# Performance work log

Hardware: AMD Instinct MI355X
Metric: run time of the kernel (lower is better)

The kernel has to match this reference:

```python
import jax, jax.numpy as jnp
import numpy as np

H = 8       # n_heads
E = 128     # embedding_size (= per-head dim)
NEG = -1000000000.0


def setup_inputs() -> dict:
    key = jax.random.key(0)
    ks = jax.random.split(key, 12)
    b, n = 8, 1024
    x = jax.random.normal(ks[0], (b, n, E), dtype=jnp.float32)
    dist = jax.random.normal(ks[1], (b, n, n), dtype=jnp.float32)
    mask = jax.random.randint(ks[2], (b, n), 0, 2).astype(jnp.float32)
    s = 1.0 / np.sqrt(E)
    Wq = jax.random.normal(ks[3], (E, H * E), dtype=jnp.float32) * s
    Wk = jax.random.normal(ks[4], (E, H * E), dtype=jnp.float32) * s
    Wv = jax.random.normal(ks[5], (E, H * E), dtype=jnp.float32) * s
    bq = jnp.zeros((H * E,), jnp.float32)
    bk = jnp.zeros((H * E,), jnp.float32)
    bv = jnp.zeros((H * E,), jnp.float32)
    Wo = jax.random.normal(ks[6], (H * E, E), dtype=jnp.float32) * (1.0 / np.sqrt(H * E))
    bo = jnp.zeros((E,), jnp.float32)
    return {"x": x, "dist": dist, "mask": mask, "Wq": Wq, "bq": bq,
            "Wk": Wk, "bk": bk, "Wv": Wv, "bv": bv, "Wo": Wo, "bo": bo}


def reference(x, dist, mask, Wq, bq, Wk, bk, Wv, bv, Wo, bo):
    b, n, e = x.shape
    scale = e ** (-0.5)
    # project and split heads: [b, n, H*E] -> [b, H, n, E]
    def heads(W, bias):
        return (x @ W + bias).reshape(b, n, H, e).transpose(0, 2, 1, 3)
    q = heads(Wq, bq) * mask[:, None, :, None]
    k = heads(Wk, bk) * mask[:, None, :, None]
    v = heads(Wv, bv) * mask[:, None, :, None]
    # scores with additive distance bias broadcast over heads
    a = jnp.einsum('bhqe,bhke->bhqk', q * scale, k) + dist[:, None, :, :]
    am = jnp.einsum('bq,bk->bqk', mask, mask)[:, None, :, :]  # [b,1,n,n]
    a = jnp.where(am == 0, NEG, a)
    a = jax.nn.softmax(a, axis=-1)
    a = jnp.where(am == 0, 0.0, a)
    y = jnp.einsum('bhqk,bhke->bhqe', a, v)
    y = y.transpose(0, 2, 1, 3).reshape(b, n, H * e)
    y = y @ Wo + bo
    return y * mask[:, :, None]
```

## Files before the change

### kernel.cpp

```cpp
#include <hip/hip_runtime.h>
#include <hip/hip_bf16.h>
#include <hip/hip_fp16.h>

#define NH 8
#define ED 128
#define NB 8
#define NN 1024

typedef __attribute__((ext_vector_type(8))) short s16x8;
typedef __attribute__((ext_vector_type(8))) __bf16 bf16x8_t;
typedef __attribute__((ext_vector_type(4))) float f32x4;
typedef __attribute__((ext_vector_type(16))) float f32x16;
typedef __attribute__((ext_vector_type(4))) unsigned int u32x4;

#define LOG2E 1.4426950408889634f
#define SINIT -23.083120654223414f

static __device__ __forceinline__ unsigned short f2bf(float f) {
    union { float f; unsigned u; } v; v.f = f;
    unsigned r = v.u + 0x7fffu + ((v.u >> 16) & 1u);
    return (unsigned short)(r >> 16);
}

static __device__ __forceinline__ f32x4 mfma16(s16x8 a, s16x8 b, f32x4 c) {
    return __builtin_amdgcn_mfma_f32_16x16x32_bf16(
        __builtin_bit_cast(bf16x8_t, a), __builtin_bit_cast(bf16x8_t, b), c, 0, 0, 0);
}

static __device__ __forceinline__ f32x16 mfma32(s16x8 a, s16x8 b, f32x16 c) {
    return __builtin_amdgcn_mfma_f32_32x32x16_bf16(
        __builtin_bit_cast(bf16x8_t, a), __builtin_bit_cast(bf16x8_t, b), c, 0, 0, 0);
}

static __device__ __forceinline__ unsigned cvtpk(float lo, float hi) {
    unsigned r;
    asm("v_cvt_pk_bf16_f32 %0, %1, %2" : "=v"(r) : "v"(lo), "v"(hi));
    return r;
}

static __device__ __forceinline__ void gll16(const void* g, void* l) {
    __builtin_amdgcn_global_load_lds((const __attribute__((address_space(1))) void*)g,
                                     (__attribute__((address_space(3))) void*)l, 16, 0, 0);
}

__global__ __launch_bounds__(256) void prep_kernel(
    const float* __restrict__ x,
    const float* __restrict__ Wq, const float* __restrict__ Wk,
    const float* __restrict__ Wv, const float* __restrict__ Wo,
    const float* __restrict__ dist,
    const float* __restrict__ mask,
    unsigned short* __restrict__ xb,
    unsigned short* __restrict__ wqt, unsigned short* __restrict__ wkt,
    unsigned short* __restrict__ wvt, unsigned short* __restrict__ wot,
    unsigned short* __restrict__ dswz) {
    int bid = blockIdx.x, tid = threadIdx.x;

    if (bid < 1024) {
        int kt = bid & 15;
        int t = bid >> 4;
        int qt = t & 7;
        int b = t >> 3;

        __shared__ float dtile[128][65];
        __shared__ float mrow[64];

        {
            int seg = tid & 15;
            int r0 = tid >> 4;
            const float* src = dist + ((size_t)b * NN + qt * 128) * NN + kt * 64;
#pragma unroll
            for (int pass = 0; pass < 8; ++pass) {
                int row = pass * 16 + r0;
                f32x4 v = *(const f32x4*)(src + (size_t)row * NN + seg * 4);
                *(f32x4*)&dtile[row][seg * 4] = v;
            }
            if (tid < 64) mrow[tid] = mask[b * NN + kt * 64 + tid];
        }
        __syncthreads();

        int h = (tid >> 5) & 1;
        int row = (tid >> 6) * 32 + (tid & 31);
#pragma unroll
        for (int c = 0; c < 4; ++c) {
            unsigned short o[8];
#pragma unroll
            for (int u = 0; u < 8; ++u) {
                int col = (c >> 1) * 32 + (c & 1) * 16 + 4 * h + (u >> 2) * 8 + (u & 3);
                float dv = dtile[row][col] * LOG2E;
                o[u] = (mrow[col] == 0.0f) ? (unsigned short)0xFBFF
                                           : __half_as_ushort(__float2half_rn(dv));
            }
            u32x4 pk;
            pk[0] = (unsigned)o[0] | ((unsigned)o[1] << 16);
            pk[1] = (unsigned)o[2] | ((unsigned)o[3] << 16);
            pk[2] = (unsigned)o[4] | ((unsigned)o[5] << 16);
            pk[3] = (unsigned)o[6] | ((unsigned)o[7] << 16);
            *(u32x4*)(dswz + ((size_t)(bid * 4 + c) * 256 + tid) * 8) = pk;
        }
        return;
    }

    if (bid < 2048) {
        int i = (bid - 1024) * 256 + tid;
        float4 v = ((const float4*)x)[i];
        unsigned long long pk = (unsigned long long)f2bf(v.x)
                              | ((unsigned long long)f2bf(v.y) << 16)
                              | ((unsigned long long)f2bf(v.z) << 32)
                              | ((unsigned long long)f2bf(v.w) << 48);
        ((unsigned long long*)xb)[i] = pk;
        return;
    }

    const float* in; unsigned short* outp; int rows_in, cols_in, i;
    if (bid < 2560)      { in = Wq; outp = wqt; rows_in = 128;  cols_in = 1024; i = (bid - 2048) * 256 + tid; }
    else if (bid < 3072) { in = Wk; outp = wkt; rows_in = 128;  cols_in = 1024; i = (bid - 2560) * 256 + tid; }
    else if (bid < 3584) { in = Wv; outp = wvt; rows_in = 128;  cols_in = 1024; i = (bid - 3072) * 256 + tid; }
    else                 { in = Wo; outp = wot; rows_in = 1024; cols_in = 128;  i = (bid - 3584) * 256 + tid; }
    int c = i / rows_in;
    int r = i - c * rows_in;
    outp[i] = f2bf(in[(size_t)r * cols_in + c]);
}

__global__ __launch_bounds__(256) void qkv_kernel(
    const unsigned short* __restrict__ xb,
    const unsigned short* __restrict__ wqt,
    const unsigned short* __restrict__ wkt,
    const unsigned short* __restrict__ wvt,
    const float* __restrict__ bq, const float* __restrict__ bk, const float* __restrict__ bv,
    unsigned short* __restrict__ q_ws,
    unsigned short* __restrict__ k_ws,
    unsigned short* __restrict__ v_ws) {
    int bid = blockIdx.x;
    int mt = bid / 24, c = bid % 24;
    int which = c >> 3;
    int c0 = (c & 7) * 128;
    int m0 = mt * 128;
    int tid = threadIdx.x;
    int w = tid >> 6, lane = tid & 63, g = lane >> 4, r15 = lane & 15;
    int wr = (w >> 1) * 64, wc = (w & 1) * 64;

    const unsigned short* wt = (which == 0) ? wqt : (which == 1) ? wkt : wvt;
    const float* bias = (which == 0) ? bq : (which == 1) ? bk : bv;

    const f32x4 fzero = {0.f, 0.f, 0.f, 0.f};
    f32x4 acc[4][4];
#pragma unroll
    for (int i = 0; i < 4; i++)
#pragma unroll
        for (int j = 0; j < 4; j++) acc[i][j] = fzero;

#pragma unroll
    for (int kf = 0; kf < 4; kf++) {
        s16x8 af[4], bfr[4];
#pragma unroll
        for (int mf = 0; mf < 4; mf++)
            af[mf] = *(const s16x8*)(xb + (size_t)(m0 + wr + mf * 16 + r15) * ED + kf * 32 + g * 8);
#pragma unroll
        for (int nf = 0; nf < 4; nf++)
            bfr[nf] = *(const s16x8*)(wt + (size_t)(c0 + wc + nf * 16 + r15) * ED + kf * 32 + g * 8);
#pragma unroll
        for (int mf = 0; mf < 4; mf++)
#pragma unroll
            for (int nf = 0; nf < 4; nf++)
                acc[mf][nf] = mfma16(af[mf], bfr[nf], acc[mf][nf]);
    }

    float scale = (which == 0) ? 0.12751741566380696f : 1.0f;

#pragma unroll
    for (int nf = 0; nf < 4; nf++) {
        int col = c0 + wc + nf * 16 + r15;
        float bv_ = bias[col];
        int hh = col >> 7, e = col & 127;
#pragma unroll
        for (int mf = 0; mf < 4; mf++) {
#pragma unroll
            for (int rr = 0; rr < 4; rr++) {
                int row = m0 + wr + mf * 16 + g * 4 + rr;
                int bb = row >> 10, n = row & 1023;
                int bh = bb * NH + hh;
                float val = (acc[mf][nf][rr] + bv_) * scale;
                if (which == 0) {
                    q_ws[((size_t)bh * NN + n) * ED + e] = f2bf(val);
                } else if (which == 1) {
                    int ktl = n >> 6, k = n & 63;
                    int slot = (e >> 4) * 128 + ((e >> 3) & 1) * 64 + (k >> 5) * 32 + (k & 31);
                    k_ws[(size_t)(bh * 16 + ktl) * 8192 + slot * 8 + (e & 7)] = f2bf(val);
                } else {
                    int ktl = n >> 6, k = n & 63;
                    int slot = (k >> 4) * 256 + ((k >> 3) & 1) * 128 + (e >> 5) * 32 + (e & 31);
                    v_ws[(size_t)(bh * 16 + ktl) * 8192 + slot * 8 + (k & 7)] = f2bf(val);
                }
            }
        }
    }
}

__global__ __launch_bounds__(256) void attn_kernel(
    const unsigned short* __restrict__ q_ws,
    const unsigned short* __restrict__ k_ws,
    const unsigned short* __restrict__ v_ws,
    const unsigned short* __restrict__ dswz,
    unsigned short* __restrict__ y_ws) {
    int p = blockIdx.x;
    int b = p & 7, r = p >> 3;
    int head = r >> 3, qt = r & 7;
    int bh = b * NH + head;
    int q0 = qt * 128;

    int tid = threadIdx.x;
    int w = tid >> 6, lane = tid & 63;
    int e31 = lane & 31, h = lane >> 5;

    __shared__ __align__(16) unsigned short Kl[2][8192];
    __shared__ __align__(16) unsigned short Vl[2][8192];

    const char* kg = (const char*)k_ws + (size_t)bh * 16 * 16384;
    const char* vg = (const char*)v_ws + (size_t)bh * 16 * 16384;
    const char* dq = (const char*)dswz + ((size_t)(b * 8 + qt) << 18);

    int qrow = q0 + w * 32 + e31;
    s16x8 qf[8];
    const unsigned short* qb = q_ws + ((size_t)bh * NN + qrow) * ED + h * 8;
#pragma unroll
    for (int es = 0; es < 8; ++es) qf[es] = *(const s16x8*)(qb + es * 16);

    const f32x16 fz16 = {0.f,0.f,0.f,0.f,0.f,0.f,0.f,0.f,0.f,0.f,0.f,0.f,0.f,0.f,0.f,0.f};
    f32x16 sini;
#pragma unroll
    for (int i = 0; i < 16; ++i) sini[i] = SINIT;
    f32x16 o0 = fz16, o1 = fz16, o2 = fz16, o3 = fz16;
    float lacc[4] = {0.f, 0.f, 0.f, 0.f};

#pragma unroll
    for (int pass = 0; pass < 4; ++pass) {
        gll16(kg + (pass * 256 + tid) * 16, (char*)&Kl[0][0] + pass * 4096 + w * 1024);
        gll16(vg + (pass * 256 + tid) * 16, (char*)&Vl[0][0] + pass * 4096 + w * 1024);
    }
    __syncthreads();

    for (int kt = 0; kt < 16; ++kt) {
        int cur = kt & 1;
        if (kt < 15) {
            const char* kn = kg + (size_t)(kt + 1) * 16384;
            const char* vn = vg + (size_t)(kt + 1) * 16384;
            char* kd = (char*)&Kl[cur ^ 1][0] + w * 1024;
            char* vd = (char*)&Vl[cur ^ 1][0] + w * 1024;
#pragma unroll
            for (int pass = 0; pass < 4; ++pass) {
                gll16(kn + (pass * 256 + tid) * 16, kd + pass * 4096);
                gll16(vn + (pass * 256 + tid) * 16, vd + pass * 4096);
            }
        }

        u32x4 dch[4];
#pragma unroll
        for (int c = 0; c < 4; ++c)
            dch[c] = *(const u32x4*)(dq + ((size_t)(kt * 4 + c) * 256 + tid) * 16);

        const char* Kp = (const char*)&Kl[cur][0] + h * 1024 + e31 * 16;
        f32x16 sA0 = sini, sA1 = sini;
        __builtin_amdgcn_s_setprio(1);
#pragma unroll
        for (int es = 0; es < 8; ++es) {
            s16x8 kb0 = *(const s16x8*)(Kp + es * 2048);
            s16x8 kb1 = *(const s16x8*)(Kp + es * 2048 + 512);
            sA0 = mfma32(kb0, qf[es], sA0);
            sA1 = mfma32(kb1, qf[es], sA1);
        }
        __builtin_amdgcn_s_setprio(0);

        float pp[32];
#pragma unroll
        for (int c = 0; c < 4; ++c) {
            float lc = 0.f;
#pragma unroll
            for (int u = 0; u < 8; ++u) {
                int i = c * 8 + u;
                unsigned wv = dch[c][u >> 1];
                float dv = __half2float(__ushort_as_half(
                    (unsigned short)((u & 1) ? (wv >> 16) : (wv & 0xffff))));
                float sv = (i < 16) ? sA0[i] : sA1[i - 16];
                float pv = __builtin_exp2f(sv + dv);
                pp[i] = pv;
                lc += pv;
            }
            lacc[c] += lc;
        }

        const char* Vp = (const char*)&Vl[cur][0] + h * 2048 + e31 * 16;
        __builtin_amdgcn_s_setprio(1);
#pragma unroll
        for (int kf = 0; kf < 2; ++kf) {
#pragma unroll
            for (int ks2 = 0; ks2 < 2; ++ks2) {
                const float* pb = &pp[kf * 16 + ks2 * 8];
                unsigned A0 = cvtpk(pb[0], pb[1]);
                unsigned A1 = cvtpk(pb[2], pb[3]);
                unsigned B0 = cvtpk(pb[4], pb[5]);
                unsigned B1 = cvtpk(pb[6], pb[7]);
                asm("v_permlane32_swap_b32 %0, %1" : "+v"(A0), "+v"(B0));
                asm("v_permlane32_swap_b32 %0, %1" : "+v"(A1), "+v"(B1));
                u32x4 pw;
                pw[0] = A0;
                pw[1] = A1;
                pw[2] = B0;
                pw[3] = B1;
                s16x8 pa = __builtin_bit_cast(s16x8, pw);
                int kstep = kf * 2 + ks2;
                const char* vp = Vp + kstep * 4096;
                o0 = mfma32(pa, *(const s16x8*)(vp), o0);
                o1 = mfma32(pa, *(const s16x8*)(vp + 512), o1);
                o2 = mfma32(pa, *(const s16x8*)(vp + 1024), o2);
                o3 = mfma32(pa, *(const s16x8*)(vp + 1536), o3);
            }
        }
        __builtin_amdgcn_s_setprio(0);
        __syncthreads();
    }

    float l_r = (lacc[0] + lacc[1]) + (lacc[2] + lacc[3]);
    float lt = l_r + __shfl_xor(l_r, 32, 64);
    float inv = (lt > 0.f) ? 1.0f / lt : 0.f;
#pragma unroll
    for (int rc = 0; rc < 4; ++rc) {
#pragma unroll
        for (int jj = 0; jj < 4; ++jj) {
            int qq = jj + 8 * rc + 4 * h;
            float iq = __shfl(inv, qq, 64);
            int row = q0 + w * 32 + qq;
            size_t base = ((size_t)b * NN + row) * (NH * ED) + head * ED + e31;
            y_ws[base]      = f2bf(o0[rc * 4 + jj] * iq);
            y_ws[base + 32] = f2bf(o1[rc * 4 + jj] * iq);
            y_ws[base + 64] = f2bf(o2[rc * 4 + jj] * iq);
            y_ws[base + 96] = f2bf(o3[rc * 4 + jj] * iq);
        }
    }
}

__global__ __launch_bounds__(256) void oproj_kernel(
    const unsigned short* __restrict__ y_ws,
    const unsigned short* __restrict__ wot,
    const float* __restrict__ bo,
    const float* __restrict__ mask,
    float* __restrict__ outp) {
    int bid = blockIdx.x;
    int mt = bid >> 1, nt = bid & 1;
    int m0 = mt * 64, c0 = nt * 64;
    int tid = threadIdx.x;
    int w = tid >> 6, lane = tid & 63, g = lane >> 4, r15 = lane & 15;

    const f32x4 fzero = {0.f, 0.f, 0.f, 0.f};
    f32x4 acc[4];
#pragma unroll
    for (int i = 0; i < 4; i++) acc[i] = fzero;

    const unsigned short* arow = y_ws + (size_t)(m0 + w * 16 + r15) * (NH * ED);
    for (int kt = 0; kt < 32; ++kt) {
        s16x8 af = *(const s16x8*)(arow + kt * 32 + g * 8);
#pragma unroll
        for (int nf = 0; nf < 4; nf++) {
            s16x8 bfr = *(const s16x8*)(wot + (size_t)(c0 + nf * 16 + r15) * (NH * ED) + kt * 32 + g * 8);
            acc[nf] = mfma16(af, bfr, acc[nf]);
        }
    }
#pragma unroll
    for (int nf = 0; nf < 4; nf++) {
        int col = c0 + nf * 16 + r15;
        float bias = bo[col];
#pragma unroll
        for (int rr = 0; rr < 4; rr++) {
            int token = m0 + w * 16 + g * 4 + rr;
            outp[(size_t)token * ED + col] = (acc[nf][rr] + bias) * mask[token];
        }
    }
}

extern "C" void kernel_launch(void* const* d_in, const int* in_sizes, int n_in,
                              void* d_out, int out_size, void* d_ws, size_t ws_size,
                              hipStream_t stream) {
    const float* x    = (const float*)d_in[0];
    const float* dist = (const float*)d_in[1];
    const float* mask = (const float*)d_in[2];
    const float* Wq   = (const float*)d_in[3];
    const float* bq   = (const float*)d_in[4];
    const float* Wk   = (const float*)d_in[5];
    const float* bk   = (const float*)d_in[6];
    const float* Wv   = (const float*)d_in[7];
    const float* bv   = (const float*)d_in[8];
    const float* Wo   = (const float*)d_in[9];
    const float* bo   = (const float*)d_in[10];
    float* outp = (float*)d_out;

    char* ws = (char*)d_ws;
    unsigned short* xb   = (unsigned short*)(ws);
    unsigned short* wqt  = (unsigned short*)(ws + (2u << 20));
    unsigned short* wkt  = (unsigned short*)(ws + (2u << 20) + (256u << 10));
    unsigned short* wvt  = (unsigned short*)(ws + (2u << 20) + (512u << 10));
    unsigned short* wot  = (unsigned short*)(ws + (2u << 20) + (768u << 10));
    unsigned short* q_ws = (unsigned short*)(ws + (3u << 20));
    unsigned short* k_ws = (unsigned short*)(ws + (19u << 20));
    unsigned short* v_ws = (unsigned short*)(ws + (35u << 20));
    unsigned short* y_ws = (unsigned short*)(ws + (51u << 20));
    unsigned short* dswz = (unsigned short*)(ws + (67u << 20));

    prep_kernel<<<4096, 256, 0, stream>>>(x, Wq, Wk, Wv, Wo, dist, mask,
                                          xb, wqt, wkt, wvt, wot, dswz);
    qkv_kernel<<<1536, 256, 0, stream>>>(xb, wqt, wkt, wvt, bq, bk, bv, q_ws, k_ws, v_ws);
    attn_kernel<<<512, 256, 0, stream>>>(q_ws, k_ws, v_ws, dswz, y_ws);
    oproj_kernel<<<256, 256, 0, stream>>>(y_ws, wot, bo, mask, outp);
}
```

Baseline: 126.4 us.

## Move dist preprocessing into QKV kernel and tile weight transposes

The dist-to-fp16 swizzle work moves out of the prep kernel and into the QKV projection launch as extra blocks, so the memory-bound dist conversion can overlap with the compute-bound QKV GEMM blocks. The dist conversion now converts to fp16 before staging through a smaller LDS tile. Weight transposes now use a 32x32 LDS tile with coalesced reads and packed 8-byte writes, replacing the strided scalar gathers. The output projection loop also gets an unroll pragma. The cost is a larger QKV kernel whose LDS footprint includes the dist tile for every block, which may lower occupancy for the GEMM blocks.

```diff
diff --git a/kernel.cpp b/kernel.cpp
--- a/kernel.cpp
+++ b/kernel.cpp
@@ -43,65 +43,16 @@
                                      (__attribute__((address_space(3))) void*)l, 16, 0, 0);
 }
 
-__global__ __launch_bounds__(256) void prep_kernel(
+__global__ __launch_bounds__(256) void prep_xw_kernel(
     const float* __restrict__ x,
     const float* __restrict__ Wq, const float* __restrict__ Wk,
     const float* __restrict__ Wv, const float* __restrict__ Wo,
-    const float* __restrict__ dist,
-    const float* __restrict__ mask,
     unsigned short* __restrict__ xb,
     unsigned short* __restrict__ wqt, unsigned short* __restrict__ wkt,
-    unsigned short* __restrict__ wvt, unsigned short* __restrict__ wot,
-    unsigned short* __restrict__ dswz) {
+    unsigned short* __restrict__ wvt, unsigned short* __restrict__ wot) {
     int bid = blockIdx.x, tid = threadIdx.x;
-
     if (bid < 1024) {
-        int kt = bid & 15;
-        int t = bid >> 4;
-        int qt = t & 7;
-        int b = t >> 3;
-
-        __shared__ float dtile[128][65];
-        __shared__ float mrow[64];
-
-        {
-            int seg = tid & 15;
-            int r0 = tid >> 4;
-            const float* src = dist + ((size_t)b * NN + qt * 128) * NN + kt * 64;
-#pragma unroll
-            for (int pass = 0; pass < 8; ++pass) {
-                int row = pass * 16 + r0;
-                f32x4 v = *(const f32x4*)(src + (size_t)row * NN + seg * 4);
-                *(f32x4*)&dtile[row][seg * 4] = v;
-            }
-            if (tid < 64) mrow[tid] = mask[b * NN + kt * 64 + tid];
-        }
-        __syncthreads();
-
-        int h = (tid >> 5) & 1;
-        int row = (tid >> 6) * 32 + (tid & 31);
-#pragma unroll
-        for (int c = 0; c < 4; ++c) {
-            unsigned short o[8];
-#pragma unroll
-            for (int u = 0; u < 8; ++u) {
-                int col = (c >> 1) * 32 + (c & 1) * 16 + 4 * h + (u >> 2) * 8 + (u & 3);
-                float dv = dtile[row][col] * LOG2E;
-                o[u] = (mrow[col] == 0.0f) ? (unsigned short)0xFBFF
-                                           : __half_as_ushort(__float2half_rn(dv));
-            }
-            u32x4 pk;
-            pk[0] = (unsigned)o[0] | ((unsigned)o[1] << 16);
-            pk[1] = (unsigned)o[2] | ((unsigned)o[3] << 16);
-            pk[2] = (unsigned)o[4] | ((unsigned)o[5] << 16);
-            pk[3] = (unsigned)o[6] | ((unsigned)o[7] << 16);
-            *(u32x4*)(dswz + ((size_t)(bid * 4 + c) * 256 + tid) * 8) = pk;
-        }
-        return;
-    }
-
-    if (bid < 2048) {
-        int i = (bid - 1024) * 256 + tid;
+        int i = bid * 256 + tid;
         float4 v = ((const float4*)x)[i];
         unsigned long long pk = (unsigned long long)f2bf(v.x)
                               | ((unsigned long long)f2bf(v.y) << 16)
@@ -110,32 +61,94 @@
         ((unsigned long long*)xb)[i] = pk;
         return;
     }
-
-    const float* in; unsigned short* outp; int rows_in, cols_in, i;
-    if (bid < 2560)      { in = Wq; outp = wqt; rows_in = 128;  cols_in = 1024; i = (bid - 2048) * 256 + tid; }
-    else if (bid < 3072) { in = Wk; outp = wkt; rows_in = 128;  cols_in = 1024; i = (bid - 2560) * 256 + tid; }
-    else if (bid < 3584) { in = Wv; outp = wvt; rows_in = 128;  cols_in = 1024; i = (bid - 3072) * 256 + tid; }
-    else                 { in = Wo; outp = wot; rows_in = 1024; cols_in = 128;  i = (bid - 3584) * 256 + tid; }
-    int c = i / rows_in;
-    int r = i - c * rows_in;
-    outp[i] = f2bf(in[(size_t)r * cols_in + c]);
-}
-
-__global__ __launch_bounds__(256) void qkv_kernel(
+    __shared__ __align__(16) float wtile[32][36];
+    int wi = bid - 1024;
+    int mat = wi >> 7, ti = wi & 127;
+    const float* in; unsigned short* outp; int rows_in, cols_in, tr0, tc0;
+    if (mat == 0)      { in = Wq; outp = wqt; rows_in = 128;  cols_in = 1024; }
+    else if (mat == 1) { in = Wk; outp = wkt; rows_in = 128;  cols_in = 1024; }
+    else if (mat == 2) { in = Wv; outp = wvt; rows_in = 128;  cols_in = 1024; }
+    else               { in = Wo; outp = wot; rows_in = 1024; cols_in = 128;  }
+    if (mat < 3) { tr0 = (ti >> 5) * 32; tc0 = (ti & 31) * 32; }
+    else         { tr0 = (ti >> 2) * 32; tc0 = (ti & 3)  * 32; }
+
+    {
+        int r = tid >> 3, cs = tid & 7;
+        f32x4 v = *(const f32x4*)(in + (size_t)(tr0 + r) * cols_in + tc0 + cs * 4);
+        *(f32x4*)&wtile[r][cs * 4] = v;
+    }
+    __syncthreads();
+    {
+        int c = tid >> 3, rs = tid & 7;
+        unsigned long long pk = (unsigned long long)f2bf(wtile[rs * 4 + 0][c])
+                              | ((unsigned long long)f2bf(wtile[rs * 4 + 1][c]) << 16)
+                              | ((unsigned long long)f2bf(wtile[rs * 4 + 2][c]) << 32)
+                              | ((unsigned long long)f2bf(wtile[rs * 4 + 3][c]) << 48);
+        *(unsigned long long*)(outp + (size_t)(tc0 + c) * rows_in + tr0 + rs * 4) = pk;
+    }
+}
+
+__global__ __launch_bounds__(256) void qkv_dist_kernel(
     const unsigned short* __restrict__ xb,
     const unsigned short* __restrict__ wqt,
     const unsigned short* __restrict__ wkt,
     const unsigned short* __restrict__ wvt,
     const float* __restrict__ bq, const float* __restrict__ bk, const float* __restrict__ bv,
+    const float* __restrict__ dist,
+    const float* __restrict__ mask,
     unsigned short* __restrict__ q_ws,
     unsigned short* __restrict__ k_ws,
-    unsigned short* __restrict__ v_ws) {
-    int bid = blockIdx.x;
-    int mt = bid / 24, c = bid % 24;
+    unsigned short* __restrict__ v_ws,
+    unsigned short* __restrict__ dswz) {
+    int bid = blockIdx.x, tid = threadIdx.x;
+
+    __shared__ __align__(16) unsigned short dt16[128][68];
+
+    if (bid < 1024) {
+        int kt = bid & 15;
+        int t = bid >> 4;
+        int qt = t & 7;
+        int b = t >> 3;
+
+        int seg = tid & 15, r0 = tid >> 4;
+        const float* src = dist + ((size_t)b * NN + qt * 128) * NN + kt * 64;
+        f32x4 m4 = *(const f32x4*)(mask + b * NN + kt * 64 + seg * 4);
+#pragma unroll
+        for (int pass = 0; pass < 8; ++pass) {
+            int row = pass * 16 + r0;
+            f32x4 d4 = *(const f32x4*)(src + (size_t)row * NN + seg * 4);
+            unsigned long long pk = 0;
+#pragma unroll
+            for (int j = 0; j < 4; ++j) {
+                unsigned short o = (m4[j] == 0.0f) ? (unsigned short)0xFBFF
+                                 : __half_as_ushort(__float2half_rn(d4[j] * LOG2E));
+                pk |= (unsigned long long)o << (16 * j);
+            }
+            *(unsigned long long*)&dt16[row][seg * 4] = pk;
+        }
+        __syncthreads();
+
+        int h = (tid >> 5) & 1;
+        int row = (tid >> 6) * 32 + (tid & 31);
+#pragma unroll
+        for (int c = 0; c < 4; ++c) {
+            int colbase = (c >> 1) * 32 + (c & 1) * 16 + 4 * h;
+            const unsigned short* rp = &dt16[row][0];
+            u32x4 pk;
+            pk[0] = *(const unsigned*)&rp[colbase];
+            pk[1] = *(const unsigned*)&rp[colbase + 2];
+            pk[2] = *(const unsigned*)&rp[colbase + 8];
+            pk[3] = *(const unsigned*)&rp[colbase + 10];
+            *(u32x4*)(dswz + ((size_t)(bid * 4 + c) * 256 + tid) * 8) = pk;
+        }
+        return;
+    }
+
+    int qb_ = bid - 1024;
+    int mt = qb_ / 24, c = qb_ % 24;
     int which = c >> 3;
     int c0 = (c & 7) * 128;
     int m0 = mt * 128;
-    int tid = threadIdx.x;
     int w = tid >> 6, lane = tid & 63, g = lane >> 4, r15 = lane & 15;
     int wr = (w >> 1) * 64, wc = (w & 1) * 64;
 
@@ -356,6 +369,7 @@
     for (int i = 0; i < 4; i++) acc[i] = fzero;
 
     const unsigned short* arow = y_ws + (size_t)(m0 + w * 16 + r15) * (NH * ED);
+#pragma unroll 4
     for (int kt = 0; kt < 32; ++kt) {
         s16x8 af = *(const s16x8*)(arow + kt * 32 + g * 8);
 #pragma unroll
@@ -404,9 +418,9 @@
     unsigned short* y_ws = (unsigned short*)(ws + (51u << 20));
     unsigned short* dswz = (unsigned short*)(ws + (67u << 20));
 
-    prep_kernel<<<4096, 256, 0, stream>>>(x, Wq, Wk, Wv, Wo, dist, mask,
-                                          xb, wqt, wkt, wvt, wot, dswz);
-    qkv_kernel<<<1536, 256, 0, stream>>>(xb, wqt, wkt, wvt, bq, bk, bv, q_ws, k_ws, v_ws);
+    prep_xw_kernel<<<1536, 256, 0, stream>>>(x, Wq, Wk, Wv, Wo, xb, wqt, wkt, wvt, wot);
+    qkv_dist_kernel<<<2560, 256, 0, stream>>>(xb, wqt, wkt, wvt, bq, bk, bv,
+                                              dist, mask, q_ws, k_ws, v_ws, dswz);
     attn_kernel<<<512, 256, 0, stream>>>(q_ws, k_ws, v_ws, dswz, y_ws);
     oproj_kernel<<<256, 256, 0, stream>>>(y_ws, wot, bo, mask, outp);
 }
```

New measurement: 128.2 us. About the same (+1.5%).
